# Kernel tuning notes

Hardware: AMD Instinct MI355X
Metric: run time of the kernel (lower is better)

## Reference

```python
import jax, jax.numpy as jnp
import numpy as np


def _avgpool(x, k):
    # x: (N, C, H, W), k divides H and W
    if k == 1:
        return x
    N, C, H, W = x.shape
    return x.reshape(N, C, H // k, k, W // k, k).mean(axis=(3, 5))


def _pairwise_sum(mu1, var1, mu2, var2):
    # mu*, var*: (N, D). Broadcast to (N, N, D), fused elementwise chain + full sum.
    d = mu1[:, None, :] - mu2[None, :, :]
    v = var1[:, None, :] + var2[None, :, :]
    return jnp.sum(jnp.exp(-0.5 * d * d / v) / jnp.sqrt(v))


def setup_inputs() -> dict:
    key = jax.random.key(0)
    k1, k2, k3, k4 = jax.random.split(key, 4)
    shape = (64, 16, 64, 64)
    return {
        "mu_a": jax.random.normal(k1, shape, dtype=jnp.float32),
        "logvar_a": jax.random.normal(k2, shape, dtype=jnp.float32),
        "mu_b": jax.random.normal(k3, shape, dtype=jnp.float32),
        "logvar_b": jax.random.normal(k4, shape, dtype=jnp.float32),
        "kern": 2,
    }


def reference(mu_a, logvar_a, mu_b, logvar_b, kern):
    k2 = float(kern * kern)
    mu_a_p = _avgpool(mu_a, kern)
    mu_b_p = _avgpool(mu_b, kern)
    var_a = _avgpool(jnp.exp(logvar_a), kern) / k2
    var_b = _avgpool(jnp.exp(logvar_b), kern) / k2

    N = mu_a_p.shape[0]
    mu_a_f = mu_a_p.reshape(N, -1)
    mu_b_f = mu_b_p.reshape(N, -1)
    var_a_f = var_a.reshape(N, -1)
    var_b_f = var_b.reshape(N, -1)

    vaa = _pairwise_sum(mu_a_f, var_a_f, mu_a_f, var_a_f)
    vab = _pairwise_sum(mu_a_f, var_a_f, mu_b_f, var_b_f)
    vbb = _pairwise_sum(mu_b_f, var_b_f, mu_b_f, var_b_f)
    return vaa + vbb - 2.0 * vab
```

## Files before the change

### kernel.cpp

```cpp
#include <hip/hip_runtime.h>

#define N_ 64
#define C_ 16
#define H_ 64
#define W_ 64

#define TRI_TILES 72
#define TILES 272
#define DCHUNKS 16
#define PAIR_BLOCKS (TILES * DCHUNKS)

#define TWO_LN2   1.3862943611198906f
#define SQRT_2LN2 1.1774100225154747f


__global__ __launch_bounds__(256) void pool_kernel(
    const float* __restrict__ mu_a, const float* __restrict__ lv_a,
    const float* __restrict__ mu_b, const float* __restrict__ lv_b,
    const int* __restrict__ kern_p, float* __restrict__ ws) {
    const int k = kern_p[0];
    const float LOG2E = 1.44269504088896f;

    if (k == 2) {
        const int Np = (N_ * C_ * H_ * W_) >> 2;
        const int Q  = Np >> 2;
        const int total = 4 * Q;
        for (int g = blockIdx.x * blockDim.x + threadIdx.x; g < total;
             g += gridDim.x * blockDim.x) {
            const int a  = g >> 18;
            const int r4 = g & (Q - 1);
            const int pw4 = (r4 & 7) << 2;
            const int t   = r4 >> 3;
            const int ph  = t & 31;
            const int nc  = t >> 5;
            const float* src = (a == 0) ? mu_a : (a == 1) ? lv_a : (a == 2) ? mu_b : lv_b;
            const bool is_var = (a & 1);
            const float* p0 = src + nc * (H_ * W_) + (ph * 2) * W_ + pw4 * 2;
            float4 r0a = *(const float4*)(p0);
            float4 r0b = *(const float4*)(p0 + 4);
            float4 r1a = *(const float4*)(p0 + W_);
            float4 r1b = *(const float4*)(p0 + W_ + 4);
            float o0, o1, o2, o3;
            if (is_var) {
#define E_(x) __builtin_amdgcn_exp2f((x) * LOG2E)
                o0 = E_(r0a.x) + E_(r0a.y) + E_(r1a.x) + E_(r1a.y);
                o1 = E_(r0a.z) + E_(r0a.w) + E_(r1a.z) + E_(r1a.w);
                o2 = E_(r0b.x) + E_(r0b.y) + E_(r1b.x) + E_(r1b.y);
                o3 = E_(r0b.z) + E_(r0b.w) + E_(r1b.z) + E_(r1b.w);
#undef E_
                const float s = (1.0f / 16.0f) * TWO_LN2;
                o0 *= s; o1 *= s; o2 *= s; o3 *= s;
            } else {
                o0 = r0a.x + r0a.y + r1a.x + r1a.y;
                o1 = r0a.z + r0a.w + r1a.z + r1a.w;
                o2 = r0b.x + r0b.y + r1b.x + r1b.y;
                o3 = r0b.z + r0b.w + r1b.z + r1b.w;
                const float s = 0.25f;
                o0 *= s; o1 *= s; o2 *= s; o3 *= s;
            }
            *(float4*)(ws + (size_t)a * Np + (size_t)r4 * 4) = make_float4(o0, o1, o2, o3);
        }
    } else {
        const int Hp = H_ / k, Wp = W_ / k;
        const int Np = N_ * C_ * Hp * Wp;
        const float inv_k2 = 1.0f / (float)(k * k);
        const float inv_k4 = inv_k2 * inv_k2 * TWO_LN2;
        const int total = 4 * Np;
        for (int p = blockIdx.x * blockDim.x + threadIdx.x; p < total;
             p += gridDim.x * blockDim.x) {
            const int a  = p / Np;
            const int r  = p - a * Np;
            const int pw = r % Wp;
            const int t1 = r / Wp;
            const int ph = t1 % Hp;
            const int nc = t1 / Hp;
            const float* src = (a == 0) ? mu_a : (a == 1) ? lv_a : (a == 2) ? mu_b : lv_b;
            const bool is_var = (a & 1);
            const int base = nc * (H_ * W_) + (ph * k) * W_ + (pw * k);
            float s = 0.0f;
            for (int dy = 0; dy < k; ++dy) {
                const float* row = src + base + dy * W_;
                for (int dx = 0; dx < k; ++dx) {
                    float x = row[dx];
                    s += is_var ? __builtin_amdgcn_exp2f(x * LOG2E) : x;
                }
            }
            ws[(size_t)a * Np + r] = s * (is_var ? inv_k4 : inv_k2);
        }
    }
}

__global__ __launch_bounds__(256) void pair_kernel(float* __restrict__ ws,
                                                   const int* __restrict__ kern_p) {
    const int k = kern_p[0];
    const int D  = C_ * (H_ / k) * (W_ / k);
    const int Np = N_ * D;

    const float* mu_a = ws;
    const float* va   = ws + (size_t)Np;
    const float* mu_b = ws + (size_t)2 * Np;
    const float* vb   = ws + (size_t)3 * Np;
    float* partials   = ws + (size_t)4 * Np;

    const int c = blockIdx.x & (DCHUNKS - 1);
    const int t = blockIdx.x >> 4;
    int set, it, jt;
    if (t >= 2 * TRI_TILES) {
        set = 2;
        const int tt = t - 2 * TRI_TILES;
        it = tt >> 3;
        jt = tt & 7;
    } else {
        set = (t >= TRI_TILES) ? 1 : 0;
        const int tt = set ? (t - TRI_TILES) : t;
        int g = 0, cum = 0;
        while (cum + (g >> 1) + 1 <= tt) { cum += (g >> 1) + 1; ++g; }
        it = g;
        jt = tt - cum;
    }
    const int i0 = it * 4, j0 = jt * 8;

    const float *mu1, *v1, *mu2, *v2;
    if (set == 0)      { mu1 = mu2 = mu_a; v1 = v2 = va; }
    else if (set == 1) { mu1 = mu2 = mu_b; v1 = v2 = vb; }
    else               { mu1 = mu_a; v1 = va; mu2 = mu_b; v2 = vb; }

#define TERM(acc, mx1, sx1, mx2, sx2)                                  \
    {                                                                  \
        float v  = (sx1) + (sx2);                                      \
        float rs = __builtin_amdgcn_rsqf(v);                           \
        float d  = (mx1) - (mx2);                                      \
        float t_ = d * rs;                                             \
        float e  = __builtin_amdgcn_exp2f(-(t_ * t_));                 \
        acc = fmaf(e, rs, acc);                                        \
    }

    float accs[4][8];
    #pragma unroll
    for (int ir = 0; ir < 4; ++ir)
        #pragma unroll
        for (int j8 = 0; j8 < 8; ++j8) accs[ir][j8] = 0.0f;

    if (D == 16384) {
        const int base = (c << 10) + ((int)threadIdx.x << 2);
        float4 im[4], iv[4];
        #pragma unroll
        for (int ir = 0; ir < 4; ++ir) {
            im[ir] = *(const float4*)(mu1 + (size_t)(i0 + ir) * 16384 + base);
            iv[ir] = *(const float4*)(v1  + (size_t)(i0 + ir) * 16384 + base);
        }
        #pragma unroll
        for (int j8 = 0; j8 < 8; ++j8) {
            const float4 jm = *(const float4*)(mu2 + (size_t)(j0 + j8) * 16384 + base);
            const float4 jv = *(const float4*)(v2  + (size_t)(j0 + j8) * 16384 + base);
            #pragma unroll
            for (int ir = 0; ir < 4; ++ir) {
                TERM(accs[ir][j8], im[ir].x, iv[ir].x, jm.x, jv.x)
                TERM(accs[ir][j8], im[ir].y, iv[ir].y, jm.y, jv.y)
                TERM(accs[ir][j8], im[ir].z, iv[ir].z, jm.z, jv.z)
                TERM(accs[ir][j8], im[ir].w, iv[ir].w, jm.w, jv.w)
            }
        }
    } else {
        const int cs = D / DCHUNKS;
        const int lo = c * cs, hi = lo + cs;
        for (int e = lo + (int)threadIdx.x; e < hi; e += 256) {
            #pragma unroll
            for (int j8 = 0; j8 < 8; ++j8) {
                const float mj = mu2[(size_t)(j0 + j8) * D + e];
                const float vj = v2 [(size_t)(j0 + j8) * D + e];
                #pragma unroll
                for (int ir = 0; ir < 4; ++ir) {
                    const float mi = mu1[(size_t)(i0 + ir) * D + e];
                    const float vi = v1 [(size_t)(i0 + ir) * D + e];
                    TERM(accs[ir][j8], mi, vi, mj, vj)
                }
            }
        }
    }
#undef TERM

    float tot = 0.0f;
    #pragma unroll
    for (int ir = 0; ir < 4; ++ir) {
        #pragma unroll
        for (int j8 = 0; j8 < 8; ++j8) {
            float w;
            if (set == 2) w = -2.0f;
            else {
                const int ii = i0 + ir, jj = j0 + j8;
                w = (jj > ii) ? 0.0f : (jj == ii) ? 1.0f : 2.0f;
            }
            tot = fmaf(w, accs[ir][j8], tot);
        }
    }
    tot *= SQRT_2LN2;

    for (int off = 32; off > 0; off >>= 1)
        tot += __shfl_down(tot, off, 64);
    __shared__ float wsum[4];
    const int lane = threadIdx.x & 63;
    const int wid  = threadIdx.x >> 6;
    if (lane == 0) wsum[wid] = tot;
    __syncthreads();
    if (threadIdx.x == 0) {
        partials[blockIdx.x] = wsum[0] + wsum[1] + wsum[2] + wsum[3];
    }
}

__global__ __launch_bounds__(256) void reduce_kernel(const float* __restrict__ ws,
                                                     const int* __restrict__ kern_p,
                                                     float* __restrict__ out) {
    const int k = kern_p[0];
    const int D  = C_ * (H_ / k) * (W_ / k);
    const int Np = N_ * D;
    const float* partials = ws + (size_t)4 * Np;

    float s = 0.0f;
    for (int p = threadIdx.x; p < PAIR_BLOCKS; p += 256) s += partials[p];
    for (int off = 32; off > 0; off >>= 1)
        s += __shfl_down(s, off, 64);
    __shared__ float wsum[4];
    const int lane = threadIdx.x & 63;
    const int wid  = threadIdx.x >> 6;
    if (lane == 0) wsum[wid] = s;
    __syncthreads();
    if (threadIdx.x == 0) out[0] = wsum[0] + wsum[1] + wsum[2] + wsum[3];
}

extern "C" void kernel_launch(void* const* d_in, const int* in_sizes, int n_in,
                              void* d_out, int out_size, void* d_ws, size_t ws_size,
                              hipStream_t stream) {
    const float* mu_a = (const float*)d_in[0];
    const float* lv_a = (const float*)d_in[1];
    const float* mu_b = (const float*)d_in[2];
    const float* lv_b = (const float*)d_in[3];
    const int*   kern = (const int*)d_in[4];
    float* out = (float*)d_out;
    float* ws  = (float*)d_ws;

    pool_kernel<<<4096, 256, 0, stream>>>(mu_a, lv_a, mu_b, lv_b, kern, ws);
    pair_kernel<<<PAIR_BLOCKS, 256, 0, stream>>>(ws, kern);
    reduce_kernel<<<1, 256, 0, stream>>>(ws, kern, out);
}
```

Before: 143.1 us.

## Fuse final reduction into pair kernel via last-block atomic counter, double D-chunks

```diff
diff --git a/kernel.cpp b/kernel.cpp
--- a/kernel.cpp
+++ b/kernel.cpp
@@ -7,7 +7,7 @@
 
 #define TRI_TILES 72
 #define TILES 272
-#define DCHUNKS 16
+#define DCHUNKS 32
 #define PAIR_BLOCKS (TILES * DCHUNKS)
 
 #define TWO_LN2   1.3862943611198906f
@@ -20,6 +20,12 @@
     const int* __restrict__ kern_p, float* __restrict__ ws) {
     const int k = kern_p[0];
     const float LOG2E = 1.44269504088896f;
+
+    if (blockIdx.x == 0 && threadIdx.x == 0) {
+        const int kk = k;
+        const int Np0 = N_ * C_ * (H_ / kk) * (W_ / kk);
+        ((int*)(ws + (size_t)4 * Np0))[PAIR_BLOCKS] = 0;
+    }
 
     if (k == 2) {
         const int Np = (N_ * C_ * H_ * W_) >> 2;
@@ -91,7 +97,8 @@
 }
 
 __global__ __launch_bounds__(256) void pair_kernel(float* __restrict__ ws,
-                                                   const int* __restrict__ kern_p) {
+                                                   const int* __restrict__ kern_p,
+                                                   float* __restrict__ out) {
     const int k = kern_p[0];
     const int D  = C_ * (H_ / k) * (W_ / k);
     const int Np = N_ * D;
@@ -101,9 +108,10 @@
     const float* mu_b = ws + (size_t)2 * Np;
     const float* vb   = ws + (size_t)3 * Np;
     float* partials   = ws + (size_t)4 * Np;
+    int*   counter    = (int*)(partials + PAIR_BLOCKS);
 
     const int c = blockIdx.x & (DCHUNKS - 1);
-    const int t = blockIdx.x >> 4;
+    const int t = blockIdx.x >> 5;
     int set, it, jt;
     if (t >= 2 * TRI_TILES) {
         set = 2;
@@ -142,28 +150,25 @@
         for (int j8 = 0; j8 < 8; ++j8) accs[ir][j8] = 0.0f;
 
     if (D == 16384) {
-        const int base = (c << 10) + ((int)threadIdx.x << 2);
-        float4 im[4], iv[4];
+        const int base = (c << 9) + ((int)threadIdx.x << 1);
+        float2 im[4], iv[4];
         #pragma unroll
         for (int ir = 0; ir < 4; ++ir) {
-            im[ir] = *(const float4*)(mu1 + (size_t)(i0 + ir) * 16384 + base);
-            iv[ir] = *(const float4*)(v1  + (size_t)(i0 + ir) * 16384 + base);
+            im[ir] = *(const float2*)(mu1 + (size_t)(i0 + ir) * 16384 + base);
+            iv[ir] = *(const float2*)(v1  + (size_t)(i0 + ir) * 16384 + base);
         }
         #pragma unroll
         for (int j8 = 0; j8 < 8; ++j8) {
-            const float4 jm = *(const float4*)(mu2 + (size_t)(j0 + j8) * 16384 + base);
-            const float4 jv = *(const float4*)(v2  + (size_t)(j0 + j8) * 16384 + base);
+            const float2 jm = *(const float2*)(mu2 + (size_t)(j0 + j8) * 16384 + base);
+            const float2 jv = *(const float2*)(v2  + (size_t)(j0 + j8) * 16384 + base);
             #pragma unroll
             for (int ir = 0; ir < 4; ++ir) {
                 TERM(accs[ir][j8], im[ir].x, iv[ir].x, jm.x, jv.x)
                 TERM(accs[ir][j8], im[ir].y, iv[ir].y, jm.y, jv.y)
-                TERM(accs[ir][j8], im[ir].z, iv[ir].z, jm.z, jv.z)
-                TERM(accs[ir][j8], im[ir].w, iv[ir].w, jm.w, jv.w)
             }
         }
     } else {
-        const int cs = D / DCHUNKS;
-        const int lo = c * cs, hi = lo + cs;
+        const int lo = (c * D) / DCHUNKS, hi = ((c + 1) * D) / DCHUNKS;
         for (int e = lo + (int)threadIdx.x; e < hi; e += 256) {
             #pragma unroll
             for (int j8 = 0; j8 < 8; ++j8) {
@@ -199,33 +204,33 @@
     for (int off = 32; off > 0; off >>= 1)
         tot += __shfl_down(tot, off, 64);
     __shared__ float wsum[4];
+    __shared__ int   lastf;
     const int lane = threadIdx.x & 63;
     const int wid  = threadIdx.x >> 6;
     if (lane == 0) wsum[wid] = tot;
     __syncthreads();
     if (threadIdx.x == 0) {
-        partials[blockIdx.x] = wsum[0] + wsum[1] + wsum[2] + wsum[3];
-    }
-}
-
-__global__ __launch_bounds__(256) void reduce_kernel(const float* __restrict__ ws,
-                                                     const int* __restrict__ kern_p,
-                                                     float* __restrict__ out) {
-    const int k = kern_p[0];
-    const int D  = C_ * (H_ / k) * (W_ / k);
-    const int Np = N_ * D;
-    const float* partials = ws + (size_t)4 * Np;
-
-    float s = 0.0f;
-    for (int p = threadIdx.x; p < PAIR_BLOCKS; p += 256) s += partials[p];
-    for (int off = 32; off > 0; off >>= 1)
-        s += __shfl_down(s, off, 64);
-    __shared__ float wsum[4];
-    const int lane = threadIdx.x & 63;
-    const int wid  = threadIdx.x >> 6;
-    if (lane == 0) wsum[wid] = s;
+        const float part = wsum[0] + wsum[1] + wsum[2] + wsum[3];
+        __hip_atomic_store(&partials[blockIdx.x], part, __ATOMIC_RELEASE,
+                           __HIP_MEMORY_SCOPE_AGENT);
+        const int old = __hip_atomic_fetch_add(counter, 1, __ATOMIC_ACQ_REL,
+                                               __HIP_MEMORY_SCOPE_AGENT);
+        lastf = (old == PAIR_BLOCKS - 1);
+    }
     __syncthreads();
-    if (threadIdx.x == 0) out[0] = wsum[0] + wsum[1] + wsum[2] + wsum[3];
+    if (lastf) {
+        float s = 0.0f;
+        for (int p = threadIdx.x; p < PAIR_BLOCKS; p += 256)
+            s += __hip_atomic_load(&partials[p], __ATOMIC_RELAXED,
+                                   __HIP_MEMORY_SCOPE_AGENT);
+        for (int off = 32; off > 0; off >>= 1)
+            s += __shfl_down(s, off, 64);
+        __syncthreads();
+        if (lane == 0) wsum[wid] = s;
+        __syncthreads();
+        if (threadIdx.x == 0)
+            out[0] = wsum[0] + wsum[1] + wsum[2] + wsum[3];
+    }
 }
 
 extern "C" void kernel_launch(void* const* d_in, const int* in_sizes, int n_in,
@@ -240,6 +245,5 @@
     float* ws  = (float*)d_ws;
 
     pool_kernel<<<4096, 256, 0, stream>>>(mu_a, lv_a, mu_b, lv_b, kern, ws);
-    pair_kernel<<<PAIR_BLOCKS, 256, 0, stream>>>(ws, kern);
-    reduce_kernel<<<1, 256, 0, stream>>>(ws, kern, out);
+    pair_kernel<<<PAIR_BLOCKS, 256, 0, stream>>>(ws, kern, out);
 }
```

New measurement: 341.7 us. +138.8%, slower.
